# Performance work log

Measured on AMD Instinct MI355X. Metric: run time of the kernel, lower is better.

## Reference

```python
import jax, jax.numpy as jnp
import numpy as np

N, D, HID, ATT, B, NC = 131072, 1024, 256, 128, 64, 2
EPS = 1e-5

def _ln(h, g, b):
    mu = jnp.mean(h, axis=-1, keepdims=True)
    var = jnp.mean((h - mu) ** 2, axis=-1, keepdims=True)
    return (h - mu) * jax.lax.rsqrt(var + EPS) * g + b

def _gelu(x):
    return jax.nn.gelu(x, approximate=False)  # torch nn.GELU default (erf)

def setup_inputs() -> dict:
    key = jax.random.key(0)
    ks = jax.random.split(key, 16)
    def w(k, shape, fan_in):
        return (jax.random.normal(k, shape, jnp.float32) / np.sqrt(fan_in)).astype(jnp.float32)
    # sorted, every bag non-empty (~equal sizes)
    segment_ids = ((jnp.arange(N) * B) // N).astype(jnp.int32)
    return {
        "x": jax.random.normal(ks[0], (N, D), jnp.float32),
        "segment_ids": segment_ids,
        "W1": w(ks[1], (D, HID), D), "b1": jnp.zeros((HID,), jnp.float32),
        "g1": jnp.ones((HID,), jnp.float32), "be1": jnp.zeros((HID,), jnp.float32),
        "W2": w(ks[2], (HID, HID), HID), "b2": jnp.zeros((HID,), jnp.float32),
        "g2": jnp.ones((HID,), jnp.float32), "be2": jnp.zeros((HID,), jnp.float32),
        "Wv": w(ks[3], (HID, ATT), HID), "bv": jnp.zeros((ATT,), jnp.float32),
        "Wu": w(ks[4], (HID, ATT), HID), "bu": jnp.zeros((ATT,), jnp.float32),
        "Ww": w(ks[5], (ATT, 1), ATT), "bw": jnp.zeros((1,), jnp.float32),
        "Wc1": w(ks[6], (HID, HID // 2), HID), "bc1": jnp.zeros((HID // 2,), jnp.float32),
        "Wc2": w(ks[7], (HID // 2, NC), HID // 2), "bc2": jnp.zeros((NC,), jnp.float32),
    }

def reference(x, segment_ids, W1, b1, g1, be1, W2, b2, g2, be2,
              Wv, bv, Wu, bu, Ww, bw, Wc1, bc1, Wc2, bc2):
    # encoder (dropout = identity at inference)
    h = _gelu(_ln(x @ W1 + b1, g1, be1))          # [N, HID]
    h = _gelu(_ln(h @ W2 + b2, g2, be2))          # [N, HID]
    # gated attention logits
    a = (jnp.tanh(h @ Wv + bv) * jax.nn.sigmoid(h @ Wu + bu)) @ Ww + bw  # [N, 1]
    a = a[:, 0]                                    # [N]
    # per-bag (segment) softmax
    m = jax.ops.segment_max(a, segment_ids, num_segments=B)             # [B]
    e = jnp.exp(a - m[segment_ids])
    s = jax.ops.segment_sum(e, segment_ids, num_segments=B)             # [B]
    attn = e / s[segment_ids]                                           # [N]
    # attention-weighted bag pooling
    z = jax.ops.segment_sum(attn[:, None] * h, segment_ids, num_segments=B)  # [B, HID]
    # classifier
    logits = _gelu(z @ Wc1 + bc1) @ Wc2 + bc2       # [B, NC]
    return logits
```

## Files before the change

### kernel.cpp

```cpp
#include <hip/hip_runtime.h>
#include <math.h>

#define N_TOK  131072
#define DIM    1024
#define HIDN   256
#define ATTN   128
#define NSEG   64
#define SEGLEN 2048
#define NCLS   2
#define EPSLN  1e-5f

typedef __attribute__((ext_vector_type(8))) short  short8;
typedef __attribute__((ext_vector_type(4))) float  f32x4;

__device__ __forceinline__ unsigned short f2bf(float f) {
    unsigned int u = __float_as_uint(f);
    u += 0x7fffu + ((u >> 16) & 1u);
    return (unsigned short)(u >> 16);
}
__device__ __forceinline__ float bf2f(unsigned short h) {
    return __uint_as_float(((unsigned int)h) << 16);
}
__device__ __forceinline__ float gelu_exact(float x) {
    return 0.5f * x * (1.0f + erff(x * 0.70710678118654752f));
}

__global__ __launch_bounds__(256) void transpose_cvt(const float* __restrict__ in,
                                                     unsigned short* __restrict__ out,
                                                     int R, int C) {
    __shared__ float t[32][33];
    const int bx = blockIdx.x * 32;
    const int by = blockIdx.y * 32;
    const int x = threadIdx.x, y = threadIdx.y;
#pragma unroll
    for (int i = 0; i < 32; i += 8) {
        int r = by + y + i, c = bx + x;
        if (r < R && c < C) t[y + i][x] = in[(size_t)r * C + c];
    }
    __syncthreads();
#pragma unroll
    for (int i = 0; i < 32; i += 8) {
        int c = bx + y + i, r = by + x;
        if (c < C && r < R) out[(size_t)c * R + r] = f2bf(t[x][y + i]);
    }
}

__global__ void build_bvu(const float* __restrict__ bv, const float* __restrict__ bu,
                          float* __restrict__ bvu) {
    int t = threadIdx.x;
    bvu[t] = (t < 128) ? bv[t] : bu[t - 128];
}

template <int K, bool AF32>
__global__ __launch_bounds__(256) void gemm_bf16(const void* __restrict__ Aptr,
                                                 const unsigned short* __restrict__ Wt,
                                                 const float* __restrict__ bias,
                                                 float* __restrict__ C) {
    __shared__ unsigned short As[64][40];
    __shared__ unsigned short Ws[256][40];
    const int tid  = threadIdx.x;
    const int wave = tid >> 6, lane = tid & 63;
    const int lr = lane & 15, lq = lane >> 4;
    const int srow = tid >> 2, skq = (tid & 3) * 8;
    const size_t row0 = (size_t)blockIdx.x * 64;

    f32x4 acc[4][4];
#pragma unroll
    for (int i = 0; i < 4; i++)
#pragma unroll
        for (int j = 0; j < 4; j++) acc[i][j] = (f32x4)0.0f;

    for (int k0 = 0; k0 < K; k0 += 32) {
        short8 aw;
        if constexpr (AF32) {
            const float* A = (const float*)Aptr;
            const float* p = &A[(row0 + srow) * K + k0 + skq];
            float4 v0 = *(const float4*)p;
            float4 v1 = *(const float4*)(p + 4);
            aw[0] = (short)f2bf(v0.x); aw[1] = (short)f2bf(v0.y);
            aw[2] = (short)f2bf(v0.z); aw[3] = (short)f2bf(v0.w);
            aw[4] = (short)f2bf(v1.x); aw[5] = (short)f2bf(v1.y);
            aw[6] = (short)f2bf(v1.z); aw[7] = (short)f2bf(v1.w);
        } else {
            const unsigned short* A = (const unsigned short*)Aptr;
            aw = *(const short8*)&A[(row0 + srow) * K + k0 + skq];
        }
        short8 ww[4];
#pragma unroll
        for (int c = 0; c < 4; c++)
            ww[c] = *(const short8*)&Wt[(size_t)(srow + 64 * c) * K + k0 + skq];

        __syncthreads();
        *(short8*)&As[srow][skq] = aw;
#pragma unroll
        for (int c = 0; c < 4; c++)
            *(short8*)&Ws[srow + 64 * c][skq] = ww[c];
        __syncthreads();

        short8 a[4], b[4];
#pragma unroll
        for (int i = 0; i < 4; i++) a[i] = *(const short8*)&As[16 * i + lr][lq * 8];
#pragma unroll
        for (int j = 0; j < 4; j++) b[j] = *(const short8*)&Ws[64 * wave + 16 * j + lr][lq * 8];
#pragma unroll
        for (int i = 0; i < 4; i++)
#pragma unroll
            for (int j = 0; j < 4; j++)
                acc[i][j] = __builtin_amdgcn_mfma_f32_16x16x32_bf16(a[i], b[j], acc[i][j], 0, 0, 0);
    }

    float bj[4];
#pragma unroll
    for (int j = 0; j < 4; j++) bj[j] = bias[wave * 64 + 16 * j + lr];
#pragma unroll
    for (int i = 0; i < 4; i++)
#pragma unroll
        for (int j = 0; j < 4; j++)
#pragma unroll
            for (int r = 0; r < 4; r++)
                C[(row0 + 16 * i + lq * 4 + r) * 256 + wave * 64 + 16 * j + lr] = acc[i][j][r] + bj[j];
}

__global__ __launch_bounds__(256) void ln_gelu_cvt(const float* __restrict__ Cin,
                                                   const float* __restrict__ g,
                                                   const float* __restrict__ be,
                                                   unsigned short* __restrict__ Hout) {
    const int row  = blockIdx.x * 4 + (threadIdx.x >> 6);
    const int lane = threadIdx.x & 63;
    float4 v = *(const float4*)&Cin[(size_t)row * HIDN + lane * 4];
    float s  = v.x + v.y + v.z + v.w;
    float sq = v.x * v.x + v.y * v.y + v.z * v.z + v.w * v.w;
#pragma unroll
    for (int o = 32; o > 0; o >>= 1) { s += __shfl_down(s, o); sq += __shfl_down(sq, o); }
    s  = __shfl(s, 0);
    sq = __shfl(sq, 0);
    const float mu  = s * (1.0f / HIDN);
    const float var = sq * (1.0f / HIDN) - mu * mu;
    const float r   = rsqrtf(var + EPSLN);
    float4 gg = *(const float4*)&g[lane * 4];
    float4 bb = *(const float4*)&be[lane * 4];
    ushort4 o4;
    o4.x = f2bf(gelu_exact((v.x - mu) * r * gg.x + bb.x));
    o4.y = f2bf(gelu_exact((v.y - mu) * r * gg.y + bb.y));
    o4.z = f2bf(gelu_exact((v.z - mu) * r * gg.z + bb.z));
    o4.w = f2bf(gelu_exact((v.w - mu) * r * gg.w + bb.w));
    *(ushort4*)&Hout[(size_t)row * HIDN + lane * 4] = o4;
}

__global__ __launch_bounds__(256) void score_act(const float* __restrict__ VU,
                                                 const float* __restrict__ Ww,
                                                 const float* __restrict__ bw,
                                                 float* __restrict__ Aout) {
    const int row  = blockIdx.x * 4 + (threadIdx.x >> 6);
    const int lane = threadIdx.x & 63;
    const float* p = VU + (size_t)row * 256;
    float2 v = *(const float2*)&p[2 * lane];
    float2 u = *(const float2*)&p[128 + 2 * lane];
    float2 w = *(const float2*)&Ww[2 * lane];
    float val = tanhf(v.x) * (1.0f / (1.0f + expf(-u.x))) * w.x
              + tanhf(v.y) * (1.0f / (1.0f + expf(-u.y))) * w.y;
#pragma unroll
    for (int o = 32; o > 0; o >>= 1) val += __shfl_down(val, o);
    if (lane == 0) Aout[row] = val + bw[0];
}

__global__ __launch_bounds__(256) void seg_softmax(float* __restrict__ A) {
    __shared__ float red[256];
    const int seg = blockIdx.x, tid = threadIdx.x;
    float* a = A + (size_t)seg * SEGLEN;
    float m = -1e30f;
#pragma unroll
    for (int c = 0; c < 8; c++) m = fmaxf(m, a[tid + 256 * c]);
    red[tid] = m; __syncthreads();
    for (int s = 128; s > 0; s >>= 1) {
        if (tid < s) red[tid] = fmaxf(red[tid], red[tid + s]);
        __syncthreads();
    }
    m = red[0]; __syncthreads();
    float e[8]; float sum = 0.0f;
#pragma unroll
    for (int c = 0; c < 8; c++) { e[c] = expf(a[tid + 256 * c] - m); sum += e[c]; }
    red[tid] = sum; __syncthreads();
    for (int s = 128; s > 0; s >>= 1) {
        if (tid < s) red[tid] += red[tid + s];
        __syncthreads();
    }
    const float inv = 1.0f / red[0];
#pragma unroll
    for (int c = 0; c < 8; c++) a[tid + 256 * c] = e[c] * inv;
}

__global__ __launch_bounds__(256) void pool_partial(const float* __restrict__ Attn,
                                                    const unsigned short* __restrict__ H,
                                                    float* __restrict__ Zp) {
    __shared__ float aw[256];
    const int tid = threadIdx.x;
    const size_t rbase = (size_t)blockIdx.x * 256;
    aw[tid] = Attn[rbase + tid];
    __syncthreads();
    const unsigned short* h = H + rbase * 256 + tid;
    float acc = 0.0f;
    for (int r = 0; r < 256; r++) acc += aw[r] * bf2f(h[(size_t)r * 256]);
    Zp[rbase + tid] = acc;
}

__global__ __launch_bounds__(256) void head_kernel(const float* __restrict__ Zp,
                                                   const float* __restrict__ Wc1,
                                                   const float* __restrict__ bc1,
                                                   const float* __restrict__ Wc2,
                                                   const float* __restrict__ bc2,
                                                   float* __restrict__ Out) {
    __shared__ float zs[256];
    __shared__ float hs[128];
    __shared__ float red[4];
    const int seg = blockIdx.x, tid = threadIdx.x;
    float z = 0.0f;
#pragma unroll
    for (int c = 0; c < 8; c++) z += Zp[((size_t)seg * 8 + c) * 256 + tid];
    zs[tid] = z;
    __syncthreads();
    if (tid < 128) {
        float acc = bc1[tid];
        for (int k = 0; k < 256; k++) acc += zs[k] * Wc1[k * 128 + tid];
        hs[tid] = gelu_exact(acc);
    }
    __syncthreads();
    const int cls = tid >> 7, j = tid & 127;
    float val = hs[j] * Wc2[j * 2 + cls];
#pragma unroll
    for (int o = 32; o > 0; o >>= 1) val += __shfl_down(val, o);
    if ((tid & 63) == 0) red[tid >> 6] = val;
    __syncthreads();
    if (tid < 2) Out[seg * 2 + tid] = red[tid * 2] + red[tid * 2 + 1] + bc2[tid];
}

extern "C" void kernel_launch(void* const* d_in, const int* in_sizes, int n_in,
                              void* d_out, int out_size, void* d_ws, size_t ws_size,
                              hipStream_t stream) {
    const float* x   = (const float*)d_in[0];
    const float* W1  = (const float*)d_in[2];
    const float* b1  = (const float*)d_in[3];
    const float* g1  = (const float*)d_in[4];
    const float* be1 = (const float*)d_in[5];
    const float* W2  = (const float*)d_in[6];
    const float* b2  = (const float*)d_in[7];
    const float* g2  = (const float*)d_in[8];
    const float* be2 = (const float*)d_in[9];
    const float* Wv  = (const float*)d_in[10];
    const float* bv  = (const float*)d_in[11];
    const float* Wu  = (const float*)d_in[12];
    const float* bu  = (const float*)d_in[13];
    const float* Ww  = (const float*)d_in[14];
    const float* bw  = (const float*)d_in[15];
    const float* Wc1 = (const float*)d_in[16];
    const float* bc1 = (const float*)d_in[17];
    const float* Wc2 = (const float*)d_in[18];
    const float* bc2 = (const float*)d_in[19];
    float* out = (float*)d_out;

    char* p = (char*)d_ws;
    float*          bufA   = (float*)p;          p += (size_t)N_TOK * HIDN * 4;
    unsigned short* h1b    = (unsigned short*)p; p += (size_t)N_TOK * HIDN * 2;
    unsigned short* h2b    = (unsigned short*)p; p += (size_t)N_TOK * HIDN * 2;
    float*          scores = (float*)p;          p += (size_t)N_TOK * 4;
    unsigned short* W1t    = (unsigned short*)p; p += (size_t)HIDN * DIM * 2;
    unsigned short* W2t    = (unsigned short*)p; p += (size_t)HIDN * HIDN * 2;
    unsigned short* Wvut   = (unsigned short*)p; p += (size_t)HIDN * HIDN * 2;
    float*          bvu    = (float*)p;          p += 256 * 4;
    float*          Zp     = (float*)p;          p += (size_t)NSEG * 8 * HIDN * 4;

    dim3 tb(32, 8);
    transpose_cvt<<<dim3(HIDN / 32, DIM / 32), tb, 0, stream>>>(W1, W1t, DIM, HIDN);
    transpose_cvt<<<dim3(HIDN / 32, HIDN / 32), tb, 0, stream>>>(W2, W2t, HIDN, HIDN);
    transpose_cvt<<<dim3(ATTN / 32, HIDN / 32), tb, 0, stream>>>(Wv, Wvut, HIDN, ATTN);
    transpose_cvt<<<dim3(ATTN / 32, HIDN / 32), tb, 0, stream>>>(Wu, Wvut + (size_t)ATTN * HIDN, HIDN, ATTN);
    build_bvu<<<1, 256, 0, stream>>>(bv, bu, bvu);

    gemm_bf16<DIM, true><<<N_TOK / 64, 256, 0, stream>>>(x, W1t, b1, bufA);
    ln_gelu_cvt<<<N_TOK / 4, 256, 0, stream>>>(bufA, g1, be1, h1b);
    gemm_bf16<HIDN, false><<<N_TOK / 64, 256, 0, stream>>>(h1b, W2t, b2, bufA);
    ln_gelu_cvt<<<N_TOK / 4, 256, 0, stream>>>(bufA, g2, be2, h2b);
    gemm_bf16<HIDN, false><<<N_TOK / 64, 256, 0, stream>>>(h2b, Wvut, bvu, bufA);
    score_act<<<N_TOK / 4, 256, 0, stream>>>(bufA, Ww, bw, scores);
    seg_softmax<<<NSEG, 256, 0, stream>>>(scores);
    pool_partial<<<NSEG * 8, 256, 0, stream>>>(scores, h2b, Zp);
    head_kernel<<<NSEG, 256, 0, stream>>>(Zp, Wc1, bc1, Wc2, bc2, out);
}
```

Measured before the change: 1.017 ms.

## Fuse LayerNorm+GELU and gated-attention scoring into GEMM epilogues

The two encoder GEMMs now carry out bias, LayerNorm and exact GELU in their epilogue. Row statistics are reduced across waves through shared memory and the bf16 result is written through a padded LDS staging tile, so the fp32 intermediate no longer makes a round trip through HBM. The V/U weights are interleaved column-wise, which lets the score GEMM pair tanh and sigmoid values via lane shuffles and reduce directly to per-token scores, removing the score_act pass. This trades more epilogue work, extra LDS (about 36KB) and a risk of lower occupancy for removing several large fp32 writes and reads and the extra launches.

```diff
diff --git a/kernel.cpp b/kernel.cpp
--- a/kernel.cpp
+++ b/kernel.cpp
@@ -7,7 +7,6 @@
 #define ATTN   128
 #define NSEG   64
 #define SEGLEN 2048
-#define NCLS   2
 #define EPSLN  1e-5f
 
 typedef __attribute__((ext_vector_type(8))) short  short8;
@@ -29,8 +28,7 @@
                                                      unsigned short* __restrict__ out,
                                                      int R, int C) {
     __shared__ float t[32][33];
-    const int bx = blockIdx.x * 32;
-    const int by = blockIdx.y * 32;
+    const int bx = blockIdx.x * 32, by = blockIdx.y * 32;
     const int x = threadIdx.x, y = threadIdx.y;
 #pragma unroll
     for (int i = 0; i < 32; i += 8) {
@@ -45,26 +43,29 @@
     }
 }
 
-__global__ void build_bvu(const float* __restrict__ bv, const float* __restrict__ bu,
-                          float* __restrict__ bvu) {
-    int t = threadIdx.x;
-    bvu[t] = (t < 128) ? bv[t] : bu[t - 128];
+__global__ __launch_bounds__(256) void build_vu(const float* __restrict__ Wv,
+                                                const float* __restrict__ Wu,
+                                                const float* __restrict__ bv,
+                                                const float* __restrict__ bu,
+                                                unsigned short* __restrict__ Wt,
+                                                float* __restrict__ bvu) {
+    const int c = blockIdx.x, k = threadIdx.x;
+    const float* src = (c & 1) ? Wu : Wv;
+    Wt[(size_t)c * HIDN + k] = f2bf(src[(size_t)k * ATTN + (c >> 1)]);
+    if (k == 0) bvu[c] = (c & 1) ? bu[c >> 1] : bv[c >> 1];
 }
 
 template <int K, bool AF32>
-__global__ __launch_bounds__(256) void gemm_bf16(const void* __restrict__ Aptr,
-                                                 const unsigned short* __restrict__ Wt,
-                                                 const float* __restrict__ bias,
-                                                 float* __restrict__ C) {
-    __shared__ unsigned short As[64][40];
-    __shared__ unsigned short Ws[256][40];
-    const int tid  = threadIdx.x;
+__device__ __forceinline__ void gemm_mainloop(const void* __restrict__ Aptr,
+                                              const unsigned short* __restrict__ Wt,
+                                              unsigned short (*As)[40],
+                                              unsigned short (*Ws)[40],
+                                              f32x4 acc[4][4],
+                                              int tid, size_t row0) {
     const int wave = tid >> 6, lane = tid & 63;
     const int lr = lane & 15, lq = lane >> 4;
     const int srow = tid >> 2, skq = (tid & 3) * 8;
-    const size_t row0 = (size_t)blockIdx.x * 64;
-
-    f32x4 acc[4][4];
+
 #pragma unroll
     for (int i = 0; i < 4; i++)
 #pragma unroll
@@ -108,6 +109,26 @@
             for (int j = 0; j < 4; j++)
                 acc[i][j] = __builtin_amdgcn_mfma_f32_16x16x32_bf16(a[i], b[j], acc[i][j], 0, 0, 0);
     }
+}
+
+template <int K, bool AF32>
+__global__ __launch_bounds__(256) void gemm_ln_gelu(const void* __restrict__ Aptr,
+                                                    const unsigned short* __restrict__ Wt,
+                                                    const float* __restrict__ bias,
+                                                    const float* __restrict__ g,
+                                                    const float* __restrict__ be,
+                                                    unsigned short* __restrict__ Hout) {
+    __shared__ __align__(16) char smem[36352];
+    unsigned short (*As)[40] = (unsigned short(*)[40])smem;
+    unsigned short (*Ws)[40] = (unsigned short(*)[40])(smem + 5120);
+    const int tid = threadIdx.x;
+    const size_t row0 = (size_t)blockIdx.x * 64;
+
+    f32x4 acc[4][4];
+    gemm_mainloop<K, AF32>(Aptr, Wt, As, Ws, acc, tid, row0);
+
+    const int wave = tid >> 6, lane = tid & 63;
+    const int lr = lane & 15, lq = lane >> 4;
 
     float bj[4];
 #pragma unroll
@@ -117,51 +138,123 @@
 #pragma unroll
         for (int j = 0; j < 4; j++)
 #pragma unroll
-            for (int r = 0; r < 4; r++)
-                C[(row0 + 16 * i + lq * 4 + r) * 256 + wave * 64 + 16 * j + lr] = acc[i][j][r] + bj[j];
-}
-
-__global__ __launch_bounds__(256) void ln_gelu_cvt(const float* __restrict__ Cin,
-                                                   const float* __restrict__ g,
-                                                   const float* __restrict__ be,
-                                                   unsigned short* __restrict__ Hout) {
-    const int row  = blockIdx.x * 4 + (threadIdx.x >> 6);
-    const int lane = threadIdx.x & 63;
-    float4 v = *(const float4*)&Cin[(size_t)row * HIDN + lane * 4];
-    float s  = v.x + v.y + v.z + v.w;
-    float sq = v.x * v.x + v.y * v.y + v.z * v.z + v.w * v.w;
-#pragma unroll
-    for (int o = 32; o > 0; o >>= 1) { s += __shfl_down(s, o); sq += __shfl_down(sq, o); }
-    s  = __shfl(s, 0);
-    sq = __shfl(sq, 0);
-    const float mu  = s * (1.0f / HIDN);
-    const float var = sq * (1.0f / HIDN) - mu * mu;
-    const float r   = rsqrtf(var + EPSLN);
-    float4 gg = *(const float4*)&g[lane * 4];
-    float4 bb = *(const float4*)&be[lane * 4];
-    ushort4 o4;
-    o4.x = f2bf(gelu_exact((v.x - mu) * r * gg.x + bb.x));
-    o4.y = f2bf(gelu_exact((v.y - mu) * r * gg.y + bb.y));
-    o4.z = f2bf(gelu_exact((v.z - mu) * r * gg.z + bb.z));
-    o4.w = f2bf(gelu_exact((v.w - mu) * r * gg.w + bb.w));
-    *(ushort4*)&Hout[(size_t)row * HIDN + lane * 4] = o4;
-}
-
-__global__ __launch_bounds__(256) void score_act(const float* __restrict__ VU,
-                                                 const float* __restrict__ Ww,
-                                                 const float* __restrict__ bw,
-                                                 float* __restrict__ Aout) {
-    const int row  = blockIdx.x * 4 + (threadIdx.x >> 6);
-    const int lane = threadIdx.x & 63;
-    const float* p = VU + (size_t)row * 256;
-    float2 v = *(const float2*)&p[2 * lane];
-    float2 u = *(const float2*)&p[128 + 2 * lane];
-    float2 w = *(const float2*)&Ww[2 * lane];
-    float val = tanhf(v.x) * (1.0f / (1.0f + expf(-u.x))) * w.x
-              + tanhf(v.y) * (1.0f / (1.0f + expf(-u.y))) * w.y;
-#pragma unroll
-    for (int o = 32; o > 0; o >>= 1) val += __shfl_down(val, o);
-    if (lane == 0) Aout[row] = val + bw[0];
+            for (int r = 0; r < 4; r++) acc[i][j][r] += bj[j];
+
+    float* sums  = (float*)(smem + 33792);
+    float* sumsq = (float*)(smem + 34816);
+    float* muA   = (float*)(smem + 35840);
+    float* rinvA = (float*)(smem + 36096);
+
+    __syncthreads();
+#pragma unroll
+    for (int i = 0; i < 4; i++)
+#pragma unroll
+        for (int r = 0; r < 4; r++) {
+            float s = 0.0f, q = 0.0f;
+#pragma unroll
+            for (int j = 0; j < 4; j++) {
+                float v = acc[i][j][r];
+                s += v; q += v * v;
+            }
+#pragma unroll
+            for (int o = 1; o < 16; o <<= 1) {
+                s += __shfl_xor(s, o);
+                q += __shfl_xor(q, o);
+            }
+            if (lr == 0) {
+                int row = 16 * i + lq * 4 + r;
+                sums[row * 4 + wave]  = s;
+                sumsq[row * 4 + wave] = q;
+            }
+        }
+    __syncthreads();
+    if (tid < 64) {
+        float S = sums[tid * 4] + sums[tid * 4 + 1] + sums[tid * 4 + 2] + sums[tid * 4 + 3];
+        float Q = sumsq[tid * 4] + sumsq[tid * 4 + 1] + sumsq[tid * 4 + 2] + sumsq[tid * 4 + 3];
+        float m_ = S * (1.0f / HIDN);
+        float v_ = Q * (1.0f / HIDN) - m_ * m_;
+        muA[tid]   = m_;
+        rinvA[tid] = rsqrtf(v_ + EPSLN);
+    }
+    __syncthreads();
+
+    unsigned short* outb = (unsigned short*)smem;
+    float gj[4], bej[4];
+#pragma unroll
+    for (int j = 0; j < 4; j++) {
+        int col = wave * 64 + 16 * j + lr;
+        gj[j] = g[col]; bej[j] = be[col];
+    }
+#pragma unroll
+    for (int i = 0; i < 4; i++)
+#pragma unroll
+        for (int r = 0; r < 4; r++) {
+            int row = 16 * i + lq * 4 + r;
+            float m_ = muA[row], rv = rinvA[row];
+#pragma unroll
+            for (int j = 0; j < 4; j++) {
+                float val = (acc[i][j][r] - m_) * rv * gj[j] + bej[j];
+                outb[row * 264 + wave * 64 + 16 * j + lr] = f2bf(gelu_exact(val));
+            }
+        }
+    __syncthreads();
+#pragma unroll
+    for (int m = 0; m < 8; m++) {
+        int u = tid + 256 * m;
+        int row = u >> 5, cb = u & 31;
+        short8 v = *(const short8*)&outb[row * 264 + cb * 8];
+        *(short8*)&Hout[(row0 + row) * 256 + cb * 8] = v;
+    }
+}
+
+template <int K>
+__global__ __launch_bounds__(256) void gemm_score(const unsigned short* __restrict__ Aptr,
+                                                  const unsigned short* __restrict__ Wt,
+                                                  const float* __restrict__ bvu,
+                                                  const float* __restrict__ Ww,
+                                                  const float* __restrict__ bw,
+                                                  float* __restrict__ Aout) {
+    __shared__ __align__(16) char smem[26624];
+    unsigned short (*As)[40] = (unsigned short(*)[40])smem;
+    unsigned short (*Ws)[40] = (unsigned short(*)[40])(smem + 5120);
+    float* ssum = (float*)(smem + 25600);
+    const int tid = threadIdx.x;
+    const size_t row0 = (size_t)blockIdx.x * 64;
+
+    f32x4 acc[4][4];
+    gemm_mainloop<K, false>(Aptr, Wt, As, Ws, acc, tid, row0);
+
+    const int wave = tid >> 6, lane = tid & 63;
+    const int lr = lane & 15, lq = lane >> 4;
+
+    float bj[4], wwj[4];
+#pragma unroll
+    for (int j = 0; j < 4; j++) {
+        bj[j]  = bvu[wave * 64 + 16 * j + lr];
+        wwj[j] = Ww[wave * 32 + 8 * j + (lr >> 1)];
+    }
+    const float bw0 = bw[0];
+
+    __syncthreads();
+#pragma unroll
+    for (int i = 0; i < 4; i++)
+#pragma unroll
+        for (int r = 0; r < 4; r++) {
+            float s = 0.0f;
+#pragma unroll
+            for (int j = 0; j < 4; j++) {
+                float v = acc[i][j][r] + bj[j];
+                float p = __shfl_xor(v, 1);
+                float c = tanhf(v) * (1.0f / (1.0f + expf(-p))) * wwj[j];
+                s += ((lr & 1) == 0) ? c : 0.0f;
+            }
+#pragma unroll
+            for (int o = 1; o < 16; o <<= 1) s += __shfl_xor(s, o);
+            if (lr == 0) ssum[(16 * i + lq * 4 + r) * 4 + wave] = s;
+        }
+    __syncthreads();
+    if (tid < 64)
+        Aout[row0 + tid] = ssum[tid * 4] + ssum[tid * 4 + 1] + ssum[tid * 4 + 2] + ssum[tid * 4 + 3] + bw0;
 }
 
 __global__ __launch_bounds__(256) void seg_softmax(float* __restrict__ A) {
@@ -259,7 +352,6 @@
     float* out = (float*)d_out;
 
     char* p = (char*)d_ws;
-    float*          bufA   = (float*)p;          p += (size_t)N_TOK * HIDN * 4;
     unsigned short* h1b    = (unsigned short*)p; p += (size_t)N_TOK * HIDN * 2;
     unsigned short* h2b    = (unsigned short*)p; p += (size_t)N_TOK * HIDN * 2;
     float*          scores = (float*)p;          p += (size_t)N_TOK * 4;
@@ -272,16 +364,11 @@
     dim3 tb(32, 8);
     transpose_cvt<<<dim3(HIDN / 32, DIM / 32), tb, 0, stream>>>(W1, W1t, DIM, HIDN);
     transpose_cvt<<<dim3(HIDN / 32, HIDN / 32), tb, 0, stream>>>(W2, W2t, HIDN, HIDN);
-    transpose_cvt<<<dim3(ATTN / 32, HIDN / 32), tb, 0, stream>>>(Wv, Wvut, HIDN, ATTN);
-    transpose_cvt<<<dim3(ATTN / 32, HIDN / 32), tb, 0, stream>>>(Wu, Wvut + (size_t)ATTN * HIDN, HIDN, ATTN);
-    build_bvu<<<1, 256, 0, stream>>>(bv, bu, bvu);
-
-    gemm_bf16<DIM, true><<<N_TOK / 64, 256, 0, stream>>>(x, W1t, b1, bufA);
-    ln_gelu_cvt<<<N_TOK / 4, 256, 0, stream>>>(bufA, g1, be1, h1b);
-    gemm_bf16<HIDN, false><<<N_TOK / 64, 256, 0, stream>>>(h1b, W2t, b2, bufA);
-    ln_gelu_cvt<<<N_TOK / 4, 256, 0, stream>>>(bufA, g2, be2, h2b);
-    gemm_bf16<HIDN, false><<<N_TOK / 64, 256, 0, stream>>>(h2b, Wvut, bvu, bufA);
-    score_act<<<N_TOK / 4, 256, 0, stream>>>(bufA, Ww, bw, scores);
+    build_vu<<<256, 256, 0, stream>>>(Wv, Wu, bv, bu, Wvut, bvu);
+
+    gemm_ln_gelu<DIM, true><<<N_TOK / 64, 256, 0, stream>>>(x, W1t, b1, g1, be1, h1b);
+    gemm_ln_gelu<HIDN, false><<<N_TOK / 64, 256, 0, stream>>>(h1b, W2t, b2, g2, be2, h2b);
+    gemm_score<HIDN><<<N_TOK / 64, 256, 0, stream>>>(h2b, Wvut, bvu, Ww, bw, scores);
     seg_softmax<<<NSEG, 256, 0, stream>>>(scores);
     pool_partial<<<NSEG * 8, 256, 0, stream>>>(scores, h2b, Zp);
     head_kernel<<<NSEG, 256, 0, stream>>>(Zp, Wc1, bc1, Wc2, bc2, out);
```

After: 1.018 ms. No clear change (+0.1%).
